# Optimization experiments

Hardware: AMD Instinct MI355X
Metric: run time of the kernel (lower is better)

## Reference

```python
import jax, jax.numpy as jnp
import numpy as np

TEMPERATURE = 0.07
NEG = -1e9  # finite stand-in for -inf; exp(-1e9) underflows to 0 in fp32, identical math


def setup_inputs() -> dict:
    key = jax.random.key(0)
    k1, k2 = jax.random.split(key)
    B, D = 8192, 128
    emb = jax.random.normal(k1, (B, D), dtype=jnp.float32)
    emb = emb / jnp.linalg.norm(emb, axis=1, keepdims=True)  # docstring: normalized embeddings
    labels = jax.random.randint(k2, (B,), 0, 2048, dtype=jnp.int64)
    return {"embeddings": emb, "labels": labels}


def reference(embeddings, labels):
    B = labels.shape[0]
    # [B, B] pairwise similarities / temperature
    sim = jnp.matmul(embeddings, embeddings.T) / TEMPERATURE
    eye = jnp.eye(B, dtype=bool)
    sim = jnp.where(eye, NEG, sim)  # mask self-similarity
    # positives: same outfit id, excluding self
    pos_mask = (labels[None, :] == labels[:, None]) & (~eye)
    # row-wise log-softmax (torch code does log_softmax over each row)
    log_probs = jax.nn.log_softmax(sim, axis=1)
    pos_count = jnp.sum(pos_mask, axis=1)  # [B]
    pos_sum = jnp.sum(jnp.where(pos_mask, log_probs, 0.0), axis=1)  # [B]
    has_pos = pos_count > 0
    row_mean = jnp.where(has_pos, pos_sum / jnp.maximum(pos_count, 1), 0.0)
    count = jnp.sum(has_pos)
    loss = -jnp.sum(row_mean) / jnp.maximum(count, 1)
    return loss
```

## Files before the change

kernel.cpp:

```cpp
#include <hip/hip_runtime.h>


#define BATCH 8192
#define DIMK  128
#define INV_T 14.285714285714286f
#define MSUB  14.285714285714286f
#define K1    20.609929155311264f
#define K2    20.609929155311264f

typedef short bf16x8 __attribute__((ext_vector_type(8)));
typedef float f32x4  __attribute__((ext_vector_type(4)));

__device__ __forceinline__ unsigned short f2bf_rne(float f) {
    unsigned u = __float_as_uint(f);
    u += 0x7FFFu + ((u >> 16) & 1u);
    return (unsigned short)(u >> 16);
}
__device__ __forceinline__ float bf2f(unsigned short b) {
    return __uint_as_float(((unsigned)b) << 16);
}

__global__ __launch_bounds__(256) void
prep_kernel(const float* __restrict__ emb, const int* __restrict__ labels,
            ushort* __restrict__ Ebf, float* __restrict__ gsum, int* __restrict__ gcnt) {
    if (blockIdx.x < 1024) {
        int i = blockIdx.x * 256 + threadIdx.x;
        float4 v = ((const float4*)emb)[i];
        ushort4 o;
        o.x = f2bf_rne(v.x); o.y = f2bf_rne(v.y);
        o.z = f2bf_rne(v.z); o.w = f2bf_rne(v.w);
        ((ushort4*)Ebf)[i] = o;
    } else {
        __shared__ int labs[BATCH];
        const int tid = threadIdx.x;
#pragma unroll
        for (int it = 0; it < 8; ++it)
            ((int4*)labs)[it * 256 + tid] = ((const int4*)labels)[it * 256 + tid];
        __syncthreads();

        const int lane = tid & 63;
        const int wid  = tid >> 6;
        const int c    = (blockIdx.x - 1024) * 4 + wid;
        float2 acc = {0.f, 0.f};
        int cnt = 0;
        int nl = labs[lane];
        for (int j0 = 0; j0 < BATCH; j0 += 64) {
            int cur = nl;
            int nidx = j0 + 64 < BATCH ? j0 + 64 : 0;
            nl = labs[nidx + lane];
            unsigned long long m = __ballot(cur == c);
            cnt += __popcll(m);
            while (m) {
                int j = __ffsll(m) - 1;
                m &= m - 1;
                float2 v = *(const float2*)(emb + (size_t)(j0 + j) * DIMK + lane * 2);
                acc.x += v.x; acc.y += v.y;
            }
        }
        *(float2*)(gsum + (size_t)c * DIMK + lane * 2) = acc;
        if (lane == 0) gcnt[c] = cnt;
    }
}

__global__ __launch_bounds__(256, 2) void
contrastive_main(const ushort* __restrict__ Ebf, float* __restrict__ zpart) {
    __shared__ __align__(16) ushort Bs[128 * DIMK];
    const int tid  = threadIdx.x;
    const int lane = tid & 63;
    const int wid  = tid >> 6;
    const int quad = lane >> 4;
    const int l16  = lane & 15;
    const int row_base = blockIdx.x * 256 + wid * 64;
    const int col_base = blockIdx.y * 128;

#pragma unroll
    for (int it = 0; it < 8; ++it) {
        int f   = it * 256 + tid;
        int col = f >> 4;
        int c   = f & 15;
        uint4 v = *(const uint4*)(Ebf + (size_t)(col_base + col) * DIMK + c * 8);
        *(uint4*)&Bs[col * DIMK + ((c ^ (col & 7)) * 8)] = v;
    }

    bf16x8 afrag[4][4];
#pragma unroll
    for (int mt = 0; mt < 4; ++mt)
#pragma unroll
        for (int kk = 0; kk < 4; ++kk)
            afrag[mt][kk] = *(const bf16x8*)(Ebf + (size_t)(row_base + mt * 16 + l16) * DIMK
                                             + kk * 32 + quad * 8);

    float zacc[16];
#pragma unroll
    for (int s = 0; s < 16; ++s) zacc[s] = 0.f;

    __syncthreads();

    for (int nt = 0; nt < 8; ++nt) {
        const int lcol = nt * 16 + l16;
        bf16x8 bfrag[4];
#pragma unroll
        for (int kk = 0; kk < 4; ++kk)
            bfrag[kk] = *(const bf16x8*)&Bs[lcol * DIMK + (((kk * 4 + quad) ^ (l16 & 7)) * 8)];

#pragma unroll
        for (int mt = 0; mt < 4; ++mt) {
            f32x4 c = {0.f, 0.f, 0.f, 0.f};
#pragma unroll
            for (int kk = 0; kk < 4; ++kk)
                c = __builtin_amdgcn_mfma_f32_16x16x32_bf16(afrag[mt][kk], bfrag[kk], c, 0, 0, 0);
#pragma unroll
            for (int r = 0; r < 4; ++r)
                zacc[mt * 4 + r] += __builtin_amdgcn_exp2f(__builtin_fmaf(c[r], K1, -K2));
        }
    }

#pragma unroll
    for (int s = 0; s < 16; ++s) {
        float z = zacc[s];
#pragma unroll
        for (int m = 1; m <= 8; m <<= 1) z += __shfl_xor(z, m, 64);
        if (l16 == 0) {
            int row = row_base + (s >> 2) * 16 + quad * 4 + (s & 3);
            zpart[(size_t)blockIdx.y * BATCH + row] = z;
        }
    }
}

__global__ __launch_bounds__(256) void
finalize1(const float* __restrict__ emb, const ushort* __restrict__ Ebf,
          const int* __restrict__ labels, const float* __restrict__ gsum,
          const int* __restrict__ gcnt, const float* __restrict__ zpart,
          float* __restrict__ bpart, int* __restrict__ bcnt) {
    __shared__ float sf[4];
    __shared__ int   si[4];
    const int lane = threadIdx.x & 63;
    const int wid  = threadIdx.x >> 6;
    const int r    = blockIdx.x * 4 + wid;
    const int lab  = labels[r];
    const int P    = gcnt[lab] - 1;

    float2 ev = *(const float2*)(emb  + (size_t)r   * DIMK + lane * 2);
    float2 gv = *(const float2*)(gsum + (size_t)lab * DIMK + lane * 2);
    unsigned bb = *(const unsigned*)(Ebf + (size_t)r * DIMK + lane * 2);
    float b0 = bf2f((unsigned short)(bb & 0xFFFF));
    float b1 = bf2f((unsigned short)(bb >> 16));

    float dotg = ev.x * gv.x + ev.y * gv.y;
    float ssd  = ev.x * ev.x + ev.y * ev.y;
    float sdbf = b0 * b0 + b1 * b1;
    float Z    = zpart[(size_t)lane * BATCH + r];

#pragma unroll
    for (int m = 1; m <= 32; m <<= 1) {
        dotg += __shfl_xor(dotg, m, 64);
        ssd  += __shfl_xor(ssd,  m, 64);
        sdbf += __shfl_xor(sdbf, m, 64);
        Z    += __shfl_xor(Z,    m, 64);
    }
    Z -= __builtin_amdgcn_exp2f(__builtin_fmaf(sdbf, K1, -K2));

    const bool has = (P > 0);
    float term = has ? ((dotg - ssd) * INV_T / (float)P - MSUB - __logf(Z)) : 0.f;
    if (lane == 0) { sf[wid] = term; si[wid] = has ? 1 : 0; }
    __syncthreads();
    if (threadIdx.x == 0) {
        bpart[blockIdx.x] = sf[0] + sf[1] + sf[2] + sf[3];
        bcnt [blockIdx.x] = si[0] + si[1] + si[2] + si[3];
    }
}

__global__ __launch_bounds__(256) void
finalize2(const float* __restrict__ bpart, const int* __restrict__ bcnt,
          float* __restrict__ out) {
    __shared__ float sf[4];
    __shared__ int   si[4];
    const int t = threadIdx.x;
    float v = 0.f; int c = 0;
#pragma unroll
    for (int k = 0; k < 8; ++k) {
        v += bpart[t + k * 256];
        c += bcnt [t + k * 256];
    }
#pragma unroll
    for (int m = 1; m <= 32; m <<= 1) {
        v += __shfl_xor(v, m, 64);
        c += __shfl_xor(c, m, 64);
    }
    if ((t & 63) == 0) { sf[t >> 6] = v; si[t >> 6] = c; }
    __syncthreads();
    if (t == 0) {
        float tot = sf[0] + sf[1] + sf[2] + sf[3];
        int cc = si[0] + si[1] + si[2] + si[3];
        out[0] = -tot / (float)(cc > 0 ? cc : 1);
    }
}

extern "C" void kernel_launch(void* const* d_in, const int* in_sizes, int n_in,
                              void* d_out, int out_size, void* d_ws, size_t ws_size,
                              hipStream_t stream) {
    const float* emb  = (const float*)d_in[0];
    const int* labels = (const int*)d_in[1];
    float* out        = (float*)d_out;

    char* ws = (char*)d_ws;
    ushort* Ebf   = (ushort*)ws;
    float*  zpart = (float*)(ws + (2u << 20));
    float*  gsum  = (float*)(ws + (4u << 20));
    int*    gcnt  = (int*)  (ws + (5u << 20));
    float*  bpart = (float*)(ws + (5u << 20) + 8192);
    int*    bcnt  = (int*)  (ws + (5u << 20) + 16384);

    prep_kernel<<<1536, 256, 0, stream>>>(emb, labels, Ebf, gsum, gcnt);
    dim3 grid(32, 64);
    contrastive_main<<<grid, 256, 0, stream>>>(Ebf, zpart);
    finalize1<<<2048, 256, 0, stream>>>(emb, Ebf, labels, gsum, gcnt, zpart, bpart, bcnt);
    finalize2<<<1, 256, 0, stream>>>(bpart, bcnt, out);
}
```

Baseline: 108.6 us.

## Exploit similarity matrix symmetry by computing only upper-triangular tile pairs

The main kernel now walks only the upper-triangular 256x256 tile pairs (528 blocks instead of 2048 128-column tiles). Each block computes its row-wise exp sums as before and also reduces column-wise exp sums, which it adds into a per-column buffer with atomics for off-diagonal tiles. The prep kernel zeroes the partial buffers, and finalize1 combines 32 row partials with the column partial. This roughly halves the MFMA and exp work, at the cost of extra shuffles, shared-memory traffic, float atomics and a coarser grid that may balance poorly across CUs.

```diff
diff --git a/kernel.cpp b/kernel.cpp
--- a/kernel.cpp
+++ b/kernel.cpp
@@ -22,9 +22,14 @@
 
 __global__ __launch_bounds__(256) void
 prep_kernel(const float* __restrict__ emb, const int* __restrict__ labels,
-            ushort* __restrict__ Ebf, float* __restrict__ gsum, int* __restrict__ gcnt) {
+            ushort* __restrict__ Ebf, float* __restrict__ gsum, int* __restrict__ gcnt,
+            float4* __restrict__ zzero) {
     if (blockIdx.x < 1024) {
         int i = blockIdx.x * 256 + threadIdx.x;
+        if (i < 67584) {
+            float4 z = {0.f, 0.f, 0.f, 0.f};
+            zzero[i] = z;
+        }
         float4 v = ((const float4*)emb)[i];
         ushort4 o;
         o.x = f2bf_rne(v.x); o.y = f2bf_rne(v.y);
@@ -63,24 +68,20 @@
 }
 
 __global__ __launch_bounds__(256, 2) void
-contrastive_main(const ushort* __restrict__ Ebf, float* __restrict__ zpart) {
+contrastive_main(const ushort* __restrict__ Ebf, float* __restrict__ zpartR,
+                 float* __restrict__ zcol) {
     __shared__ __align__(16) ushort Bs[128 * DIMK];
+    __shared__ float cpart[4][256];
     const int tid  = threadIdx.x;
     const int lane = tid & 63;
     const int wid  = tid >> 6;
     const int quad = lane >> 4;
     const int l16  = lane & 15;
-    const int row_base = blockIdx.x * 256 + wid * 64;
-    const int col_base = blockIdx.y * 128;
-
-#pragma unroll
-    for (int it = 0; it < 8; ++it) {
-        int f   = it * 256 + tid;
-        int col = f >> 4;
-        int c   = f & 15;
-        uint4 v = *(const uint4*)(Ebf + (size_t)(col_base + col) * DIMK + c * 8);
-        *(uint4*)&Bs[col * DIMK + ((c ^ (col & 7)) * 8)] = v;
-    }
+
+    int b = blockIdx.x, ti = 0;
+    while (b >= 32 - ti) { b -= 32 - ti; ++ti; }
+    const int tj = ti + b;
+    const int row_base = ti * 256 + wid * 64;
 
     bf16x8 afrag[4][4];
 #pragma unroll
@@ -94,24 +95,44 @@
 #pragma unroll
     for (int s = 0; s < 16; ++s) zacc[s] = 0.f;
 
-    __syncthreads();
-
-    for (int nt = 0; nt < 8; ++nt) {
-        const int lcol = nt * 16 + l16;
-        bf16x8 bfrag[4];
-#pragma unroll
-        for (int kk = 0; kk < 4; ++kk)
-            bfrag[kk] = *(const bf16x8*)&Bs[lcol * DIMK + (((kk * 4 + quad) ^ (l16 & 7)) * 8)];
-
-#pragma unroll
-        for (int mt = 0; mt < 4; ++mt) {
-            f32x4 c = {0.f, 0.f, 0.f, 0.f};
+#pragma unroll
+    for (int half = 0; half < 2; ++half) {
+        const int col_base = tj * 256 + half * 128;
+        __syncthreads();
+#pragma unroll
+        for (int it = 0; it < 8; ++it) {
+            int f   = it * 256 + tid;
+            int col = f >> 4;
+            int c   = f & 15;
+            uint4 v = *(const uint4*)(Ebf + (size_t)(col_base + col) * DIMK + c * 8);
+            *(uint4*)&Bs[col * DIMK + ((c ^ (col & 7)) * 8)] = v;
+        }
+        __syncthreads();
+
+        for (int nt = 0; nt < 8; ++nt) {
+            const int lcol = nt * 16 + l16;
+            bf16x8 bfrag[4];
 #pragma unroll
             for (int kk = 0; kk < 4; ++kk)
-                c = __builtin_amdgcn_mfma_f32_16x16x32_bf16(afrag[mt][kk], bfrag[kk], c, 0, 0, 0);
-#pragma unroll
-            for (int r = 0; r < 4; ++r)
-                zacc[mt * 4 + r] += __builtin_amdgcn_exp2f(__builtin_fmaf(c[r], K1, -K2));
+                bfrag[kk] = *(const bf16x8*)&Bs[lcol * DIMK + (((kk * 4 + quad) ^ (l16 & 7)) * 8)];
+
+            float csum = 0.f;
+#pragma unroll
+            for (int mt = 0; mt < 4; ++mt) {
+                f32x4 c = {0.f, 0.f, 0.f, 0.f};
+#pragma unroll
+                for (int kk = 0; kk < 4; ++kk)
+                    c = __builtin_amdgcn_mfma_f32_16x16x32_bf16(afrag[mt][kk], bfrag[kk], c, 0, 0, 0);
+#pragma unroll
+                for (int r = 0; r < 4; ++r) {
+                    float e = __builtin_amdgcn_exp2f(__builtin_fmaf(c[r], K1, -K2));
+                    zacc[mt * 4 + r] += e;
+                    csum += e;
+                }
+            }
+            csum += __shfl_xor(csum, 16, 64);
+            csum += __shfl_xor(csum, 32, 64);
+            if (quad == 0) cpart[wid][half * 128 + nt * 16 + l16] = csum;
         }
     }
 
@@ -122,15 +143,22 @@
         for (int m = 1; m <= 8; m <<= 1) z += __shfl_xor(z, m, 64);
         if (l16 == 0) {
             int row = row_base + (s >> 2) * 16 + quad * 4 + (s & 3);
-            zpart[(size_t)blockIdx.y * BATCH + row] = z;
-        }
+            zpartR[(size_t)tj * BATCH + row] = z;
+        }
+    }
+
+    __syncthreads();
+    if (ti != tj) {
+        float s = cpart[0][tid] + cpart[1][tid] + cpart[2][tid] + cpart[3][tid];
+        atomicAdd(&zcol[tj * 256 + tid], s);
     }
 }
 
 __global__ __launch_bounds__(256) void
 finalize1(const float* __restrict__ emb, const ushort* __restrict__ Ebf,
           const int* __restrict__ labels, const float* __restrict__ gsum,
-          const int* __restrict__ gcnt, const float* __restrict__ zpart,
+          const int* __restrict__ gcnt, const float* __restrict__ zpartR,
+          const float* __restrict__ zcol,
           float* __restrict__ bpart, int* __restrict__ bcnt) {
     __shared__ float sf[4];
     __shared__ int   si[4];
@@ -149,7 +177,9 @@
     float dotg = ev.x * gv.x + ev.y * gv.y;
     float ssd  = ev.x * ev.x + ev.y * ev.y;
     float sdbf = b0 * b0 + b1 * b1;
-    float Z    = zpart[(size_t)lane * BATCH + r];
+    float Z = 0.f;
+    if (lane < 32)       Z = zpartR[(size_t)lane * BATCH + r];
+    else if (lane == 32) Z = zcol[r];
 
 #pragma unroll
     for (int m = 1; m <= 32; m <<= 1) {
@@ -204,16 +234,16 @@
     float* out        = (float*)d_out;
 
     char* ws = (char*)d_ws;
-    ushort* Ebf   = (ushort*)ws;
-    float*  zpart = (float*)(ws + (2u << 20));
-    float*  gsum  = (float*)(ws + (4u << 20));
-    int*    gcnt  = (int*)  (ws + (5u << 20));
-    float*  bpart = (float*)(ws + (5u << 20) + 8192);
-    int*    bcnt  = (int*)  (ws + (5u << 20) + 16384);
-
-    prep_kernel<<<1536, 256, 0, stream>>>(emb, labels, Ebf, gsum, gcnt);
-    dim3 grid(32, 64);
-    contrastive_main<<<grid, 256, 0, stream>>>(Ebf, zpart);
-    finalize1<<<2048, 256, 0, stream>>>(emb, Ebf, labels, gsum, gcnt, zpart, bpart, bcnt);
+    ushort* Ebf    = (ushort*)ws;
+    float*  zpartR = (float*)(ws + (2u << 20));
+    float*  zcol   = (float*)(ws + (3u << 20));
+    float*  gsum   = (float*)(ws + (4u << 20));
+    int*    gcnt   = (int*)  (ws + (5u << 20));
+    float*  bpart  = (float*)(ws + (5u << 20) + 8192);
+    int*    bcnt   = (int*)  (ws + (5u << 20) + 16384);
+
+    prep_kernel<<<1536, 256, 0, stream>>>(emb, labels, Ebf, gsum, gcnt, (float4*)zpartR);
+    contrastive_main<<<528, 256, 0, stream>>>(Ebf, zpartR, zcol);
+    finalize1<<<2048, 256, 0, stream>>>(emb, Ebf, labels, gsum, gcnt, zpartR, zcol, bpart, bcnt);
     finalize2<<<1, 256, 0, stream>>>(bpart, bcnt, out);
 }
```

Measured after the change: 128.0 us. 17.9% more time.
